# Kernel optimization log

Measured on AMD Instinct MI355X. Metric: run time of the kernel, lower is better.

The kernel has to match this reference:

```python
import jax, jax.numpy as jnp
import numpy as np

DIM = 1024
NUM_HEADS = 16
HEAD_DIM = DIM // NUM_HEADS
SCALING = HEAD_DIM ** (-0.5)


def setup_inputs() -> dict:
    key = jax.random.key(0)
    ks = jax.random.split(key, 9)
    B, S = 2, 2048
    s = DIM ** -0.5  # ~ torch Linear init scale
    inp = {
        "x": jax.random.normal(ks[0], (B, S, DIM), dtype=jnp.float32),
        "wq": jax.random.uniform(ks[1], (DIM, DIM), jnp.float32, -s, s),
        "bq": jax.random.uniform(ks[2], (DIM,), jnp.float32, -s, s),
        "wk": jax.random.uniform(ks[3], (DIM, DIM), jnp.float32, -s, s),
        "bk": jax.random.uniform(ks[4], (DIM,), jnp.float32, -s, s),
        "wv": jax.random.uniform(ks[5], (DIM, DIM), jnp.float32, -s, s),
        "bv": jax.random.uniform(ks[6], (DIM,), jnp.float32, -s, s),
        "wo": jax.random.uniform(ks[7], (DIM, DIM), jnp.float32, -s, s),
        "bo": jax.random.uniform(ks[8], (DIM,), jnp.float32, -s, s),
    }
    return inp


def reference(x, wq, bq, wk, bk, wv, bv, wo, bo):
    B, S, D = x.shape
    # projections (weights stored [out,in] like torch Linear -> x @ W.T + b)
    q = (x @ wq.T + bq).reshape(B, S, NUM_HEADS, HEAD_DIM)
    k = (x @ wk.T + bk).reshape(B, S, NUM_HEADS, HEAD_DIM)
    v = (x @ wv.T + bv).reshape(B, S, NUM_HEADS, HEAD_DIM)
    # [B,H,S,S] scores, scaled
    scores = jnp.einsum("bqhd,bkhd->bhqk", q, k) * SCALING
    attn = jax.nn.softmax(scores, axis=-1)
    # dropout p=0.0 (eval): identity
    out = jnp.einsum("bhqk,bkhd->bqhd", attn, v).reshape(B, S, D)
    return out @ wo.T + bo
```

## Files before the change

kernel.cpp:

```cpp
#include <hip/hip_runtime.h>

#define DIM 1024
#define NHEADS 16
#define HDIM 64
#define BATCH 2
#define SEQ 2048
#define MTOT (BATCH*SEQ)
#define QSCALE 0.18033688011112042f
#define XN ((size_t)MTOT*DIM)
#define WN ((size_t)DIM*DIM)

typedef __attribute__((ext_vector_type(8))) short short8;
typedef __attribute__((ext_vector_type(4))) float f32x4;
typedef __attribute__((ext_vector_type(16))) float f32x16;
typedef __attribute__((ext_vector_type(2))) int int2v;

static __device__ __forceinline__ unsigned short bf16rne(float f) {
    unsigned u = __builtin_bit_cast(unsigned, f);
    return (unsigned short)((u + 0x7fffu + ((u >> 16) & 1u)) >> 16);
}

static __device__ __forceinline__ void gld16(const void* g, void* l) {
    __builtin_amdgcn_global_load_lds((const __attribute__((address_space(1))) void*)g,
                                     (__attribute__((address_space(3))) void*)l, 16, 0, 0);
}

static __device__ __forceinline__ f32x16 mfma32(short8 a, short8 b, f32x16 c) {
    return __builtin_amdgcn_mfma_f32_32x32x16_bf16(a, b, c, 0, 0, 0);
}

__global__ __launch_bounds__(256)
void prep(const float* __restrict__ x, const float* __restrict__ wq, const float* __restrict__ wk,
          const float* __restrict__ wv, const float* __restrict__ wo, unsigned short* __restrict__ dst)
{
    const size_t i = ((size_t)blockIdx.x*256 + threadIdx.x)*8;
    const float* s; size_t o;
    if (i < XN)           { s = x;  o = i; }
    else if (i < XN+WN)   { s = wq; o = i - XN; }
    else if (i < XN+2*WN) { s = wk; o = i - XN - WN; }
    else if (i < XN+3*WN) { s = wv; o = i - XN - 2*WN; }
    else                  { s = wo; o = i - XN - 3*WN; }
    float4 a = *(const float4*)(s + o);
    float4 b = *(const float4*)(s + o + 4);
    uint4 w;
    w.x = (unsigned)bf16rne(a.x) | ((unsigned)bf16rne(a.y) << 16);
    w.y = (unsigned)bf16rne(a.z) | ((unsigned)bf16rne(a.w) << 16);
    w.z = (unsigned)bf16rne(b.x) | ((unsigned)bf16rne(b.y) << 16);
    w.w = (unsigned)bf16rne(b.z) | ((unsigned)bf16rne(b.w) << 16);
    *(uint4*)&dst[i] = w;
}

__global__ __launch_bounds__(256)
void gemm_qkv(const unsigned short* __restrict__ A,
              const unsigned short* __restrict__ W0, const unsigned short* __restrict__ W1,
              const unsigned short* __restrict__ W2,
              const float* __restrict__ b0, const float* __restrict__ b1, const float* __restrict__ b2,
              unsigned short* __restrict__ o0, unsigned short* __restrict__ o1, unsigned short* __restrict__ o2)
{
    __shared__ __align__(16) unsigned short As[3][4096];
    __shared__ __align__(16) unsigned short Bs[3][4096];
    const int t = threadIdx.x, wid = t >> 6, lane = t & 63;
    const int lr = lane & 15, lg = lane >> 4;
    const int bid = blockIdx.y * 24 + blockIdx.x;
    const int swz = (bid & 7) * 96 + (bid >> 3);
    const int sx = swz % 24, sy = swz / 24;
    const int widx = sx >> 3;
    const int n0 = (sx & 7) << 7;
    const int m0 = sy << 7;
    const unsigned short* W = widx == 0 ? W0 : (widx == 1 ? W1 : W2);
    const float* bias        = widx == 0 ? b0 : (widx == 1 ? b1 : b2);
    const float scale        = widx == 0 ? QSCALE : 1.0f;
    unsigned short* out      = widx == 0 ? o0 : (widx == 1 ? o1 : o2);

    const int wm = wid >> 1, wn = wid & 1;
    const int f0 = 2*wid, f1 = f0 + 1;
    const unsigned short* Ag0 = A + (size_t)(m0 + f0*16 + lr)*DIM + lg*8;
    const unsigned short* Ag1 = A + (size_t)(m0 + f1*16 + lr)*DIM + lg*8;
    const unsigned short* Bg0 = W + (size_t)(n0 + f0*16 + lr)*DIM + lg*8;
    const unsigned short* Bg1 = W + (size_t)(n0 + f1*16 + lr)*DIM + lg*8;

    auto stage = [&](int tt, int slot) {
        const int ko = tt * 32;
        gld16(Ag0 + ko, &As[slot][f0*512]); gld16(Ag1 + ko, &As[slot][f1*512]);
        gld16(Bg0 + ko, &Bs[slot][f0*512]); gld16(Bg1 + ko, &Bs[slot][f1*512]);
    };

    f32x4 acc[4][4] = {};
    stage(0, 0); stage(1, 1);
    int c0 = 0, c1 = 1, c2 = 2;

    for (int it = 0; it < DIM/32; ++it) {
        if (it < DIM/32 - 2) { asm volatile("s_waitcnt vmcnt(4)" ::: "memory"); }
        else                 { asm volatile("s_waitcnt vmcnt(0)" ::: "memory"); }
        __builtin_amdgcn_s_barrier();
        short8 af[4], bf[4];
        #pragma unroll
        for (int i = 0; i < 4; ++i) af[i] = *(const short8*)&As[c0][(wm*4+i)*512 + lane*8];
        #pragma unroll
        for (int i = 0; i < 4; ++i) bf[i] = *(const short8*)&Bs[c0][(wn*4+i)*512 + lane*8];
        if (it + 2 < DIM/32) stage(it + 2, c2);
        __builtin_amdgcn_s_setprio(1);
        #pragma unroll
        for (int mb = 0; mb < 4; ++mb)
            #pragma unroll
            for (int nb = 0; nb < 4; ++nb)
                acc[mb][nb] = __builtin_amdgcn_mfma_f32_16x16x32_bf16(af[mb], bf[nb], acc[mb][nb], 0, 0, 0);
        __builtin_amdgcn_s_setprio(0);
        const int tmp = c0; c0 = c1; c1 = c2; c2 = tmp;
    }

    #pragma unroll
    for (int nb = 0; nb < 4; ++nb) {
        const int col = n0 + wn*64 + nb*16 + lr;
        const float bv = bias[col];
        #pragma unroll
        for (int mb = 0; mb < 4; ++mb) {
            #pragma unroll
            for (int j = 0; j < 4; ++j) {
                const int row = m0 + wm*64 + mb*16 + lg*4 + j;
                out[(size_t)row*DIM + col] = bf16rne((acc[mb][nb][j] + bv) * scale);
            }
        }
    }
}

__global__ __launch_bounds__(256)
void gemm_o(const unsigned short* __restrict__ A, const unsigned short* __restrict__ W,
            const float* __restrict__ bias, float* __restrict__ fo)
{
    __shared__ __align__(16) unsigned short As[3][2048];
    __shared__ __align__(16) unsigned short Bs[3][4096];
    const int t = threadIdx.x, wid = t >> 6, lane = t & 63;
    const int lr = lane & 15, lg = lane >> 4;
    const int bid = blockIdx.y * 8 + blockIdx.x;
    const int swz = (bid & 7) * 64 + (bid >> 3);
    const int n0 = (swz & 7) << 7;
    const int m0 = (swz >> 3) << 6;
    const int wm = wid >> 1, wn = wid & 1;

    const int fa = wid;
    const int g0 = 2*wid, g1 = g0 + 1;
    const unsigned short* Ag  = A + (size_t)(m0 + fa*16 + lr)*DIM + lg*8;
    const unsigned short* Bg0 = W + (size_t)(n0 + g0*16 + lr)*DIM + lg*8;
    const unsigned short* Bg1 = W + (size_t)(n0 + g1*16 + lr)*DIM + lg*8;

    auto stage = [&](int tt, int slot) {
        const int ko = tt * 32;
        gld16(Ag + ko, &As[slot][fa*512]);
        gld16(Bg0 + ko, &Bs[slot][g0*512]); gld16(Bg1 + ko, &Bs[slot][g1*512]);
    };

    f32x4 acc[2][4] = {};
    stage(0, 0); stage(1, 1);
    int c0 = 0, c1 = 1, c2 = 2;

    for (int it = 0; it < DIM/32; ++it) {
        if (it < DIM/32 - 2) { asm volatile("s_waitcnt vmcnt(3)" ::: "memory"); }
        else                 { asm volatile("s_waitcnt vmcnt(0)" ::: "memory"); }
        __builtin_amdgcn_s_barrier();
        short8 af[2], bf[4];
        #pragma unroll
        for (int i = 0; i < 2; ++i) af[i] = *(const short8*)&As[c0][(wm*2+i)*512 + lane*8];
        #pragma unroll
        for (int i = 0; i < 4; ++i) bf[i] = *(const short8*)&Bs[c0][(wn*4+i)*512 + lane*8];
        if (it + 2 < DIM/32) stage(it + 2, c2);
        __builtin_amdgcn_s_setprio(1);
        #pragma unroll
        for (int mb = 0; mb < 2; ++mb)
            #pragma unroll
            for (int nb = 0; nb < 4; ++nb)
                acc[mb][nb] = __builtin_amdgcn_mfma_f32_16x16x32_bf16(af[mb], bf[nb], acc[mb][nb], 0, 0, 0);
        __builtin_amdgcn_s_setprio(0);
        const int tmp = c0; c0 = c1; c1 = c2; c2 = tmp;
    }

    #pragma unroll
    for (int nb = 0; nb < 4; ++nb) {
        const int col = n0 + wn*64 + nb*16 + lr;
        const float bv = bias[col];
        #pragma unroll
        for (int mb = 0; mb < 2; ++mb) {
            #pragma unroll
            for (int j = 0; j < 4; ++j) {
                const int row = m0 + wm*32 + mb*16 + lg*4 + j;
                fo[(size_t)row*DIM + col] = acc[mb][nb][j] + bv;
            }
        }
    }
}

__global__ __launch_bounds__(256)
void pack_kv(const unsigned short* __restrict__ Kg, const unsigned short* __restrict__ V,
             unsigned short* __restrict__ Kp, unsigned short* __restrict__ Vp)
{
    __shared__ unsigned short tile[64][66];
    const int t  = threadIdx.x;
    const int st = blockIdx.x;
    const int bh = blockIdx.y;
    const int isV = blockIdx.z;
    const int b = bh >> 4, h = bh & 15;
    const unsigned short* src = isV ? V : Kg;
    unsigned short* dstb = (isV ? Vp : Kp) + ((size_t)bh*32 + st)*4096;
    const int sr = t >> 3;
    const int dc = (t & 7) * 8;

    #pragma unroll
    for (int r = 0; r < 2; ++r) {
        const int s = r*32 + sr;
        short8 v = *(const short8*)(src + (size_t)(b*SEQ + st*64 + s)*DIM + h*HDIM + dc);
        #pragma unroll
        for (int e = 0; e < 8; ++e) tile[s][dc + e] = (unsigned short)v[e];
    }
    __syncthreads();
    #pragma unroll
    for (int r = 0; r < 2; ++r) {
        const int idx = t + r*256;
        const int fr = idx >> 6, ln = idx & 63;
        short8 ov;
        if (isV) {
            const int s0 = (fr & 3)*16 + (ln >> 5)*8;
            const int d  = (fr >> 2)*32 + (ln & 31);
            #pragma unroll
            for (int e = 0; e < 8; ++e) ov[e] = (short)tile[s0 + e][d];
        } else {
            const int key = (fr >> 2)*32 + (ln & 31);
            const int d0  = (fr & 3)*16 + (ln >> 5)*8;
            #pragma unroll
            for (int e = 0; e < 8; ++e) ov[e] = (short)tile[key][d0 + e];
        }
        *(short8*)(dstb + fr*512 + ln*8) = ov;
    }
}

struct PA { short8 p[4]; };

static __device__ __forceinline__ PA softmax_pack(const f32x16& s0, const f32x16& s1, float& lsum) {
    float rsum = 0.f;
    unsigned pw0[4][2], pw1[4][2];
    #pragma unroll
    for (int r1 = 0; r1 < 4; ++r1)
        #pragma unroll
        for (int tt = 0; tt < 2; ++tt) {
            float pa_ = __builtin_amdgcn_exp2f(s0[4*r1+2*tt]);
            float pb_ = __builtin_amdgcn_exp2f(s0[4*r1+2*tt+1]);
            float pc_ = __builtin_amdgcn_exp2f(s1[4*r1+2*tt]);
            float pd_ = __builtin_amdgcn_exp2f(s1[4*r1+2*tt+1]);
            rsum += (pa_ + pb_) + (pc_ + pd_);
            asm("v_cvt_pk_bf16_f32 %0, %1, %2" : "=v"(pw0[r1][tt]) : "v"(pa_), "v"(pb_));
            asm("v_cvt_pk_bf16_f32 %0, %1, %2" : "=v"(pw1[r1][tt]) : "v"(pc_), "v"(pd_));
        }
    rsum += __shfl_xor(rsum, 32);
    lsum += rsum;
    PA r;
    #pragma unroll
    for (int ss = 0; ss < 4; ++ss) {
        union { short8 s8; unsigned u[4]; } pu;
        #pragma unroll
        for (int tt = 0; tt < 2; ++tt) {
            const unsigned a = (ss >> 1) ? pw1[2*(ss&1)][tt]   : pw0[2*(ss&1)][tt];
            const unsigned b = (ss >> 1) ? pw1[2*(ss&1)+1][tt] : pw0[2*(ss&1)+1][tt];
            int2v sw = __builtin_amdgcn_permlane32_swap((int)a, (int)b, false, false);
            pu.u[tt]     = (unsigned)sw[0];
            pu.u[2 + tt] = (unsigned)sw[1];
        }
        r.p[ss] = pu.s8;
    }
    return r;
}

__global__ __launch_bounds__(256)
void attn_mfma2(const unsigned short* __restrict__ Q, const unsigned short* __restrict__ Kp,
                const unsigned short* __restrict__ Vp, unsigned short* __restrict__ O)
{
    __shared__ __align__(16) unsigned short Ks[4][4096];
    __shared__ __align__(16) unsigned short Vs[4][4096];
    const int t = threadIdx.x, wid = t >> 6, lane = t & 63;
    const int l31 = lane & 31, h = lane >> 5;
    const int bid = blockIdx.y * 16 + blockIdx.x;
    const int swz = (bid & 7) * 64 + (bid >> 3);
    const int qt = swz & 15, bh = swz >> 4;
    const int b = bh >> 4, hh = bh & 15;
    const size_t qkbase = (size_t)b*SEQ*DIM + (size_t)hh*HDIM;
    const unsigned short* Qb = Q + qkbase;
    unsigned short*       Ob = O + qkbase;
    const int q0 = qt*128 + wid*32;

    short8 qf[4];
    #pragma unroll
    for (int ds = 0; ds < 4; ++ds)
        qf[ds] = *(const short8*)&Qb[(size_t)(q0 + l31)*DIM + ds*16 + h*8];

    const int f0 = 2*wid, f1 = f0 + 1;
    const unsigned short* Kg0 = Kp + (size_t)bh*32*4096 + f0*512 + lane*8;
    const unsigned short* Kg1 = Kg0 + 512;
    const unsigned short* Vg0 = Vp + (size_t)bh*32*4096 + f0*512 + lane*8;
    const unsigned short* Vg1 = Vg0 + 512;

    auto stage = [&](int tn) {
        const size_t ko = (size_t)tn * 4096;
        const int bb = tn & 3;
        gld16(Kg0 + ko, &Ks[bb][f0*512]); gld16(Kg1 + ko, &Ks[bb][f1*512]);
        gld16(Vg0 + ko, &Vs[bb][f0*512]); gld16(Vg1 + ko, &Vs[bb][f1*512]);
    };

    f32x16 ctx0 = {}, ctx1 = {};
    float lsum = 0.0f;

    stage(0); stage(1);

    const int NW = SEQ/128;
    for (int w = 0; w < NW; ++w) {
        const int t0 = 2*w;
        const int ba = t0 & 3, bb2 = (t0+1) & 3;
        const bool more = (w + 1 < NW);

        if (more) { asm volatile("s_waitcnt vmcnt(4)" ::: "memory"); }
        else      { asm volatile("s_waitcnt vmcnt(0)" ::: "memory"); }
        __builtin_amdgcn_s_barrier();
        if (more) stage(t0 + 2);

        f32x16 s0a = {}, s1a = {};
        __builtin_amdgcn_s_setprio(1);
        #pragma unroll
        for (int ds = 0; ds < 4; ++ds) {
            short8 kf0 = *(const short8*)&Ks[ba][ds*512 + lane*8];
            short8 kf1 = *(const short8*)&Ks[ba][(4+ds)*512 + lane*8];
            s0a = mfma32(kf0, qf[ds], s0a);
            s1a = mfma32(kf1, qf[ds], s1a);
        }
        __builtin_amdgcn_s_setprio(0);

        PA pa = softmax_pack(s0a, s1a, lsum);

        if (more) { asm volatile("s_waitcnt vmcnt(4)" ::: "memory"); }
        else      { asm volatile("s_waitcnt vmcnt(0)" ::: "memory"); }
        __builtin_amdgcn_s_barrier();
        if (more) stage(t0 + 3);

        f32x16 s0b = {}, s1b = {};
        __builtin_amdgcn_s_setprio(1);
        #pragma unroll
        for (int ds = 0; ds < 4; ++ds) {
            short8 kf0 = *(const short8*)&Ks[bb2][ds*512 + lane*8];
            short8 kf1 = *(const short8*)&Ks[bb2][(4+ds)*512 + lane*8];
            s0b = mfma32(kf0, qf[ds], s0b);
            s1b = mfma32(kf1, qf[ds], s1b);
        }
        #pragma unroll
        for (int ss = 0; ss < 4; ++ss) {
            short8 vf0 = *(const short8*)&Vs[ba][ss*512 + lane*8];
            short8 vf1 = *(const short8*)&Vs[ba][(4+ss)*512 + lane*8];
            ctx0 = mfma32(pa.p[ss], vf0, ctx0);
            ctx1 = mfma32(pa.p[ss], vf1, ctx1);
        }
        __builtin_amdgcn_s_setprio(0);

        PA pb = softmax_pack(s0b, s1b, lsum);

        __builtin_amdgcn_s_setprio(1);
        #pragma unroll
        for (int ss = 0; ss < 4; ++ss) {
            short8 vf0 = *(const short8*)&Vs[bb2][ss*512 + lane*8];
            short8 vf1 = *(const short8*)&Vs[bb2][(4+ss)*512 + lane*8];
            ctx0 = mfma32(pb.p[ss], vf0, ctx0);
            ctx1 = mfma32(pb.p[ss], vf1, ctx1);
        }
        __builtin_amdgcn_s_setprio(0);
    }

    const float linv = 1.0f / lsum;
    #pragma unroll
    for (int r = 0; r < 16; ++r) {
        const int qrow = (r&3) + 8*(r>>2) + 4*h;
        const float nm = __shfl(linv, qrow);
        unsigned short* p = &Ob[(size_t)(q0 + qrow)*DIM + l31];
        p[0]  = bf16rne(ctx0[r] * nm);
        p[32] = bf16rne(ctx1[r] * nm);
    }
}

extern "C" void kernel_launch(void* const* d_in, const int* in_sizes, int n_in,
                              void* d_out, int out_size, void* d_ws, size_t ws_size,
                              hipStream_t stream) {
    const float* x  = (const float*)d_in[0];
    const float* wq = (const float*)d_in[1];
    const float* bq = (const float*)d_in[2];
    const float* wk = (const float*)d_in[3];
    const float* bk = (const float*)d_in[4];
    const float* wv = (const float*)d_in[5];
    const float* bv = (const float*)d_in[6];
    const float* wo = (const float*)d_in[7];
    const float* bo = (const float*)d_in[8];
    float* out = (float*)d_out;

    unsigned short* Xb  = (unsigned short*)d_ws;
    unsigned short* Wqb = Xb  + XN;
    unsigned short* Wkb = Wqb + WN;
    unsigned short* Wvb = Wkb + WN;
    unsigned short* Wob = Wvb + WN;
    unsigned short* Qb  = Wob + WN;
    unsigned short* Kb  = Qb  + XN;
    unsigned short* Vb  = Kb  + XN;
    unsigned short* Vpb = Vb  + XN;
    unsigned short* Kpb = Xb;
    unsigned short* Cb  = Vb;

    prep<<<4096, 256, 0, stream>>>(x, wq, wk, wv, wo, Xb);

    gemm_qkv<<<dim3(24, 32), 256, 0, stream>>>(Xb, Wqb, Wkb, Wvb, bq, bk, bv, Qb, Kb, Vb);

    pack_kv<<<dim3(SEQ/64, BATCH*NHEADS, 2), 256, 0, stream>>>(Kb, Vb, Kpb, Vpb);
    attn_mfma2<<<dim3(SEQ/128, BATCH*NHEADS), 256, 0, stream>>>(Qb, Kpb, Vpb, Cb);

    gemm_o<<<dim3(8, 64), 256, 0, stream>>>(Cb, Wob, bo, out);
}
```

Measured before the change: 139.7 us.

## Split attention over two key halves and merge partials in a combine kernel

The attention kernel now splits the key/value sequence into two halves along a new grid z-dimension. Each block writes unnormalized bf16 partial contexts and row sums to workspace. A new combine kernel adds the two partials, normalizes them and writes the context tensor for the output projection. This doubles the number of attention blocks to fill more of the GPU, at the cost of an extra launch and extra global traffic. The K/V staging also shrinks from four buffers to double buffering with a full vmcnt(0) wait each tile, which reduces load/compute overlap.

```diff
diff --git a/kernel.cpp b/kernel.cpp
--- a/kernel.cpp
+++ b/kernel.cpp
@@ -18,6 +18,9 @@
 static __device__ __forceinline__ unsigned short bf16rne(float f) {
     unsigned u = __builtin_bit_cast(unsigned, f);
     return (unsigned short)((u + 0x7fffu + ((u >> 16) & 1u)) >> 16);
+}
+static __device__ __forceinline__ float bf2f(unsigned short u) {
+    return __builtin_bit_cast(float, (unsigned)u << 16);
 }
 
 static __device__ __forceinline__ void gld16(const void* g, void* l) {
@@ -269,20 +272,20 @@
 }
 
 __global__ __launch_bounds__(256)
-void attn_mfma2(const unsigned short* __restrict__ Q, const unsigned short* __restrict__ Kp,
-                const unsigned short* __restrict__ Vp, unsigned short* __restrict__ O)
-{
-    __shared__ __align__(16) unsigned short Ks[4][4096];
-    __shared__ __align__(16) unsigned short Vs[4][4096];
+void attn_ks(const unsigned short* __restrict__ Q, const unsigned short* __restrict__ Kp,
+             const unsigned short* __restrict__ Vp,
+             unsigned short* __restrict__ Pc, float* __restrict__ Pl)
+{
+    __shared__ __align__(16) unsigned short Ks[2][4096];
+    __shared__ __align__(16) unsigned short Vs[2][4096];
     const int t = threadIdx.x, wid = t >> 6, lane = t & 63;
     const int l31 = lane & 31, h = lane >> 5;
     const int bid = blockIdx.y * 16 + blockIdx.x;
     const int swz = (bid & 7) * 64 + (bid >> 3);
     const int qt = swz & 15, bh = swz >> 4;
+    const int kz = blockIdx.z;
     const int b = bh >> 4, hh = bh & 15;
-    const size_t qkbase = (size_t)b*SEQ*DIM + (size_t)hh*HDIM;
-    const unsigned short* Qb = Q + qkbase;
-    unsigned short*       Ob = O + qkbase;
+    const unsigned short* Qb = Q + (size_t)b*SEQ*DIM + (size_t)hh*HDIM;
     const int q0 = qt*128 + wid*32;
 
     short8 qf[4];
@@ -291,92 +294,92 @@
         qf[ds] = *(const short8*)&Qb[(size_t)(q0 + l31)*DIM + ds*16 + h*8];
 
     const int f0 = 2*wid, f1 = f0 + 1;
-    const unsigned short* Kg0 = Kp + (size_t)bh*32*4096 + f0*512 + lane*8;
+    const size_t kvbase = (size_t)(bh*32 + kz*16)*4096;
+    const unsigned short* Kg0 = Kp + kvbase + f0*512 + lane*8;
     const unsigned short* Kg1 = Kg0 + 512;
-    const unsigned short* Vg0 = Vp + (size_t)bh*32*4096 + f0*512 + lane*8;
+    const unsigned short* Vg0 = Vp + kvbase + f0*512 + lane*8;
     const unsigned short* Vg1 = Vg0 + 512;
 
     auto stage = [&](int tn) {
         const size_t ko = (size_t)tn * 4096;
-        const int bb = tn & 3;
-        gld16(Kg0 + ko, &Ks[bb][f0*512]); gld16(Kg1 + ko, &Ks[bb][f1*512]);
-        gld16(Vg0 + ko, &Vs[bb][f0*512]); gld16(Vg1 + ko, &Vs[bb][f1*512]);
+        const int sl = tn & 1;
+        gld16(Kg0 + ko, &Ks[sl][f0*512]); gld16(Kg1 + ko, &Ks[sl][f1*512]);
+        gld16(Vg0 + ko, &Vs[sl][f0*512]); gld16(Vg1 + ko, &Vs[sl][f1*512]);
     };
 
     f32x16 ctx0 = {}, ctx1 = {};
     float lsum = 0.0f;
 
-    stage(0); stage(1);
-
-    const int NW = SEQ/128;
-    for (int w = 0; w < NW; ++w) {
-        const int t0 = 2*w;
-        const int ba = t0 & 3, bb2 = (t0+1) & 3;
-        const bool more = (w + 1 < NW);
-
-        if (more) { asm volatile("s_waitcnt vmcnt(4)" ::: "memory"); }
-        else      { asm volatile("s_waitcnt vmcnt(0)" ::: "memory"); }
+    stage(0);
+
+    for (int tn = 0; tn < 16; ++tn) {
+        const int sl = tn & 1;
+        asm volatile("s_waitcnt vmcnt(0)" ::: "memory");
         __builtin_amdgcn_s_barrier();
-        if (more) stage(t0 + 2);
-
-        f32x16 s0a = {}, s1a = {};
+        if (tn + 1 < 16) stage(tn + 1);
+
+        f32x16 s0 = {}, s1 = {};
         __builtin_amdgcn_s_setprio(1);
         #pragma unroll
         for (int ds = 0; ds < 4; ++ds) {
-            short8 kf0 = *(const short8*)&Ks[ba][ds*512 + lane*8];
-            short8 kf1 = *(const short8*)&Ks[ba][(4+ds)*512 + lane*8];
-            s0a = mfma32(kf0, qf[ds], s0a);
-            s1a = mfma32(kf1, qf[ds], s1a);
+            short8 kf0 = *(const short8*)&Ks[sl][ds*512 + lane*8];
+            short8 kf1 = *(const short8*)&Ks[sl][(4+ds)*512 + lane*8];
+            s0 = mfma32(kf0, qf[ds], s0);
+            s1 = mfma32(kf1, qf[ds], s1);
         }
         __builtin_amdgcn_s_setprio(0);
 
-        PA pa = softmax_pack(s0a, s1a, lsum);
-
-        if (more) { asm volatile("s_waitcnt vmcnt(4)" ::: "memory"); }
-        else      { asm volatile("s_waitcnt vmcnt(0)" ::: "memory"); }
-        __builtin_amdgcn_s_barrier();
-        if (more) stage(t0 + 3);
-
-        f32x16 s0b = {}, s1b = {};
+        PA pa = softmax_pack(s0, s1, lsum);
+
         __builtin_amdgcn_s_setprio(1);
         #pragma unroll
-        for (int ds = 0; ds < 4; ++ds) {
-            short8 kf0 = *(const short8*)&Ks[bb2][ds*512 + lane*8];
-            short8 kf1 = *(const short8*)&Ks[bb2][(4+ds)*512 + lane*8];
-            s0b = mfma32(kf0, qf[ds], s0b);
-            s1b = mfma32(kf1, qf[ds], s1b);
-        }
-        #pragma unroll
         for (int ss = 0; ss < 4; ++ss) {
-            short8 vf0 = *(const short8*)&Vs[ba][ss*512 + lane*8];
-            short8 vf1 = *(const short8*)&Vs[ba][(4+ss)*512 + lane*8];
+            short8 vf0 = *(const short8*)&Vs[sl][ss*512 + lane*8];
+            short8 vf1 = *(const short8*)&Vs[sl][(4+ss)*512 + lane*8];
             ctx0 = mfma32(pa.p[ss], vf0, ctx0);
             ctx1 = mfma32(pa.p[ss], vf1, ctx1);
         }
         __builtin_amdgcn_s_setprio(0);
-
-        PA pb = softmax_pack(s0b, s1b, lsum);
-
-        __builtin_amdgcn_s_setprio(1);
-        #pragma unroll
-        for (int ss = 0; ss < 4; ++ss) {
-            short8 vf0 = *(const short8*)&Vs[bb2][ss*512 + lane*8];
-            short8 vf1 = *(const short8*)&Vs[bb2][(4+ss)*512 + lane*8];
-            ctx0 = mfma32(pb.p[ss], vf0, ctx0);
-            ctx1 = mfma32(pb.p[ss], vf1, ctx1);
-        }
-        __builtin_amdgcn_s_setprio(0);
-    }
-
-    const float linv = 1.0f / lsum;
+    }
+
+    const size_t prow = ((size_t)kz*32 + bh)*SEQ + q0;
     #pragma unroll
     for (int r = 0; r < 16; ++r) {
         const int qrow = (r&3) + 8*(r>>2) + 4*h;
-        const float nm = __shfl(linv, qrow);
-        unsigned short* p = &Ob[(size_t)(q0 + qrow)*DIM + l31];
-        p[0]  = bf16rne(ctx0[r] * nm);
-        p[32] = bf16rne(ctx1[r] * nm);
-    }
+        unsigned short* p = &Pc[(prow + qrow)*64 + l31];
+        p[0]  = bf16rne(ctx0[r]);
+        p[32] = bf16rne(ctx1[r]);
+    }
+    if (lane < 32)
+        Pl[(size_t)kz*(32*SEQ) + (size_t)bh*SEQ + q0 + l31] = lsum;
+}
+
+__global__ __launch_bounds__(256)
+void combine(const unsigned short* __restrict__ Pc, const float* __restrict__ Pl,
+             unsigned short* __restrict__ Cb)
+{
+    const int i = blockIdx.x*256 + threadIdx.x;
+    const int row = i >> 3;
+    const int dc = (i & 7) * 8;
+    const float inv = 1.0f / (Pl[row] + Pl[32*SEQ + row]);
+    short8 a = *(const short8*)&Pc[(size_t)row*64 + dc];
+    short8 c = *(const short8*)&Pc[((size_t)32*SEQ + row)*64 + dc];
+    const int bh = row >> 11, s = row & (SEQ-1);
+    unsigned short* o = &Cb[((size_t)(bh>>4)*SEQ + s)*DIM + (bh&15)*HDIM + dc];
+    uint4 w;
+    float v0 = (bf2f((unsigned short)a[0]) + bf2f((unsigned short)c[0]))*inv;
+    float v1 = (bf2f((unsigned short)a[1]) + bf2f((unsigned short)c[1]))*inv;
+    float v2 = (bf2f((unsigned short)a[2]) + bf2f((unsigned short)c[2]))*inv;
+    float v3 = (bf2f((unsigned short)a[3]) + bf2f((unsigned short)c[3]))*inv;
+    float v4 = (bf2f((unsigned short)a[4]) + bf2f((unsigned short)c[4]))*inv;
+    float v5 = (bf2f((unsigned short)a[5]) + bf2f((unsigned short)c[5]))*inv;
+    float v6 = (bf2f((unsigned short)a[6]) + bf2f((unsigned short)c[6]))*inv;
+    float v7 = (bf2f((unsigned short)a[7]) + bf2f((unsigned short)c[7]))*inv;
+    w.x = (unsigned)bf16rne(v0) | ((unsigned)bf16rne(v1) << 16);
+    w.y = (unsigned)bf16rne(v2) | ((unsigned)bf16rne(v3) << 16);
+    w.z = (unsigned)bf16rne(v4) | ((unsigned)bf16rne(v5) << 16);
+    w.w = (unsigned)bf16rne(v6) | ((unsigned)bf16rne(v7) << 16);
+    *(uint4*)o = w;
 }
 
 extern "C" void kernel_launch(void* const* d_in, const int* in_sizes, int n_in,
@@ -403,14 +406,19 @@
     unsigned short* Vb  = Kb  + XN;
     unsigned short* Vpb = Vb  + XN;
     unsigned short* Kpb = Xb;
-    unsigned short* Cb  = Vb;
+    unsigned short* Pc  = Kb;
+    float*          Pl  = (float*)Wqb;
+    unsigned short* Cb  = Qb;
 
     prep<<<4096, 256, 0, stream>>>(x, wq, wk, wv, wo, Xb);
 
     gemm_qkv<<<dim3(24, 32), 256, 0, stream>>>(Xb, Wqb, Wkb, Wvb, bq, bk, bv, Qb, Kb, Vb);
 
     pack_kv<<<dim3(SEQ/64, BATCH*NHEADS, 2), 256, 0, stream>>>(Kb, Vb, Kpb, Vpb);
-    attn_mfma2<<<dim3(SEQ/128, BATCH*NHEADS), 256, 0, stream>>>(Qb, Kpb, Vpb, Cb);
+
+    attn_ks<<<dim3(16, BATCH*NHEADS, 2), 256, 0, stream>>>(Qb, Kpb, Vpb, Pc, Pl);
+
+    combine<<<2048, 256, 0, stream>>>(Pc, Pl, Cb);
 
     gemm_o<<<dim3(8, 64), 256, 0, stream>>>(Cb, Wob, bo, out);
 }
```

Result: slower. 149.2 us (+6.9%).

## Fuse K/V fragment packing into QKV GEMM epilogue via shared-memory transpose

Applied to the files above, without the earlier changes.

The QKV projection epilogue for K and V now stages the bias-added bf16 tile in shared memory, reusing the pipeline buffers. It then writes directly in the packed per-head fragment layout that the attention kernel consumes, so the separate pack_kv kernel is removed. This saves one launch and a full read and write of K and V through global memory. In exchange the GEMM epilogue gains two block barriers and strided, possibly bank-conflicting shared-memory reads, and the workspace aliasing changes so the attention output reuses the X buffer.

```diff
diff --git a/kernel.cpp b/kernel.cpp
--- a/kernel.cpp
+++ b/kernel.cpp
@@ -57,8 +57,9 @@
               const float* __restrict__ b0, const float* __restrict__ b1, const float* __restrict__ b2,
               unsigned short* __restrict__ o0, unsigned short* __restrict__ o1, unsigned short* __restrict__ o2)
 {
-    __shared__ __align__(16) unsigned short As[3][4096];
-    __shared__ __align__(16) unsigned short Bs[3][4096];
+    __shared__ __align__(16) unsigned short smem[24576];
+    #define AS(s) (smem + (s)*4096)
+    #define BS(s) (smem + 12288 + (s)*4096)
     const int t = threadIdx.x, wid = t >> 6, lane = t & 63;
     const int lr = lane & 15, lg = lane >> 4;
     const int bid = blockIdx.y * 24 + blockIdx.x;
@@ -69,8 +70,6 @@
     const int m0 = sy << 7;
     const unsigned short* W = widx == 0 ? W0 : (widx == 1 ? W1 : W2);
     const float* bias        = widx == 0 ? b0 : (widx == 1 ? b1 : b2);
-    const float scale        = widx == 0 ? QSCALE : 1.0f;
-    unsigned short* out      = widx == 0 ? o0 : (widx == 1 ? o1 : o2);
 
     const int wm = wid >> 1, wn = wid & 1;
     const int f0 = 2*wid, f1 = f0 + 1;
@@ -81,8 +80,8 @@
 
     auto stage = [&](int tt, int slot) {
         const int ko = tt * 32;
-        gld16(Ag0 + ko, &As[slot][f0*512]); gld16(Ag1 + ko, &As[slot][f1*512]);
-        gld16(Bg0 + ko, &Bs[slot][f0*512]); gld16(Bg1 + ko, &Bs[slot][f1*512]);
+        gld16(Ag0 + ko, AS(slot) + f0*512); gld16(Ag1 + ko, AS(slot) + f1*512);
+        gld16(Bg0 + ko, BS(slot) + f0*512); gld16(Bg1 + ko, BS(slot) + f1*512);
     };
 
     f32x4 acc[4][4] = {};
@@ -95,9 +94,9 @@
         __builtin_amdgcn_s_barrier();
         short8 af[4], bf[4];
         #pragma unroll
-        for (int i = 0; i < 4; ++i) af[i] = *(const short8*)&As[c0][(wm*4+i)*512 + lane*8];
-        #pragma unroll
-        for (int i = 0; i < 4; ++i) bf[i] = *(const short8*)&Bs[c0][(wn*4+i)*512 + lane*8];
+        for (int i = 0; i < 4; ++i) af[i] = *(const short8*)(AS(c0) + (wm*4+i)*512 + lane*8);
+        #pragma unroll
+        for (int i = 0; i < 4; ++i) bf[i] = *(const short8*)(BS(c0) + (wn*4+i)*512 + lane*8);
         if (it + 2 < DIM/32) stage(it + 2, c2);
         __builtin_amdgcn_s_setprio(1);
         #pragma unroll
@@ -109,19 +108,65 @@
         const int tmp = c0; c0 = c1; c1 = c2; c2 = tmp;
     }
 
-    #pragma unroll
-    for (int nb = 0; nb < 4; ++nb) {
-        const int col = n0 + wn*64 + nb*16 + lr;
-        const float bv = bias[col];
-        #pragma unroll
-        for (int mb = 0; mb < 4; ++mb) {
+    if (widx == 0) {
+        #pragma unroll
+        for (int nb = 0; nb < 4; ++nb) {
+            const int col = n0 + wn*64 + nb*16 + lr;
+            const float bv = bias[col];
             #pragma unroll
-            for (int j = 0; j < 4; ++j) {
-                const int row = m0 + wm*64 + mb*16 + lg*4 + j;
-                out[(size_t)row*DIM + col] = bf16rne((acc[mb][nb][j] + bv) * scale);
+            for (int mb = 0; mb < 4; ++mb) {
+                #pragma unroll
+                for (int j = 0; j < 4; ++j) {
+                    const int row = m0 + wm*64 + mb*16 + lg*4 + j;
+                    o0[(size_t)row*DIM + col] = bf16rne((acc[mb][nb][j] + bv) * QSCALE);
+                }
             }
         }
-    }
+    } else {
+        unsigned short* outp = (widx == 1) ? o1 : o2;
+        const int isV = (widx == 2);
+        __syncthreads();
+        unsigned short (*tile)[136] = (unsigned short (*)[136])smem;
+        #pragma unroll
+        for (int nb = 0; nb < 4; ++nb) {
+            const int col = wn*64 + nb*16 + lr;
+            const float bv = bias[n0 + col];
+            #pragma unroll
+            for (int mb = 0; mb < 4; ++mb) {
+                #pragma unroll
+                for (int j = 0; j < 4; ++j)
+                    tile[wm*64 + mb*16 + lg*4 + j][col] = bf16rne(acc[mb][nb][j] + bv);
+            }
+        }
+        __syncthreads();
+        const int bb  = m0 >> 11;
+        const int kt0 = (m0 & (SEQ-1)) >> 6;
+        const int hh0 = n0 >> 6;
+        #pragma unroll
+        for (int shot = 0; shot < 8; ++shot) {
+            const int idx = t + shot*256;
+            const int tid = idx >> 9;
+            const int fr  = (idx >> 6) & 7;
+            const int ln  = idx & 63;
+            const int ktl = tid & 1, hhl = tid >> 1;
+            short8 ov;
+            if (isV) {
+                const int r0 = ktl*64 + (fr & 3)*16 + (ln >> 5)*8;
+                const int c  = hhl*64 + (fr >> 2)*32 + (ln & 31);
+                #pragma unroll
+                for (int e = 0; e < 8; ++e) ov[e] = (short)tile[r0 + e][c];
+            } else {
+                const int r  = ktl*64 + (fr >> 2)*32 + (ln & 31);
+                const int cc = hhl*64 + (fr & 3)*16 + (ln >> 5)*8;
+                ov = *(const short8*)&tile[r][cc];
+            }
+            unsigned short* dst = outp
+                + ((size_t)((bb*NHEADS + hh0 + hhl)*32 + kt0 + ktl))*4096 + fr*512 + ln*8;
+            *(short8*)dst = ov;
+        }
+    }
+    #undef AS
+    #undef BS
 }
 
 __global__ __launch_bounds__(256)
@@ -186,49 +231,6 @@
                 fo[(size_t)row*DIM + col] = acc[mb][nb][j] + bv;
             }
         }
-    }
-}
-
-__global__ __launch_bounds__(256)
-void pack_kv(const unsigned short* __restrict__ Kg, const unsigned short* __restrict__ V,
-             unsigned short* __restrict__ Kp, unsigned short* __restrict__ Vp)
-{
-    __shared__ unsigned short tile[64][66];
-    const int t  = threadIdx.x;
-    const int st = blockIdx.x;
-    const int bh = blockIdx.y;
-    const int isV = blockIdx.z;
-    const int b = bh >> 4, h = bh & 15;
-    const unsigned short* src = isV ? V : Kg;
-    unsigned short* dstb = (isV ? Vp : Kp) + ((size_t)bh*32 + st)*4096;
-    const int sr = t >> 3;
-    const int dc = (t & 7) * 8;
-
-    #pragma unroll
-    for (int r = 0; r < 2; ++r) {
-        const int s = r*32 + sr;
-        short8 v = *(const short8*)(src + (size_t)(b*SEQ + st*64 + s)*DIM + h*HDIM + dc);
-        #pragma unroll
-        for (int e = 0; e < 8; ++e) tile[s][dc + e] = (unsigned short)v[e];
-    }
-    __syncthreads();
-    #pragma unroll
-    for (int r = 0; r < 2; ++r) {
-        const int idx = t + r*256;
-        const int fr = idx >> 6, ln = idx & 63;
-        short8 ov;
-        if (isV) {
-            const int s0 = (fr & 3)*16 + (ln >> 5)*8;
-            const int d  = (fr >> 2)*32 + (ln & 31);
-            #pragma unroll
-            for (int e = 0; e < 8; ++e) ov[e] = (short)tile[s0 + e][d];
-        } else {
-            const int key = (fr >> 2)*32 + (ln & 31);
-            const int d0  = (fr & 3)*16 + (ln >> 5)*8;
-            #pragma unroll
-            for (int e = 0; e < 8; ++e) ov[e] = (short)tile[key][d0 + e];
-        }
-        *(short8*)(dstb + fr*512 + ln*8) = ov;
     }
 }
 
@@ -399,17 +401,14 @@
     unsigned short* Wvb = Wkb + WN;
     unsigned short* Wob = Wvb + WN;
     unsigned short* Qb  = Wob + WN;
-    unsigned short* Kb  = Qb  + XN;
-    unsigned short* Vb  = Kb  + XN;
-    unsigned short* Vpb = Vb  + XN;
-    unsigned short* Kpb = Xb;
-    unsigned short* Cb  = Vb;
+    unsigned short* Kpb = Qb  + XN;
+    unsigned short* Vpb = Kpb + XN;
+    unsigned short* Cb  = Xb;
 
     prep<<<4096, 256, 0, stream>>>(x, wq, wk, wv, wo, Xb);
 
-    gemm_qkv<<<dim3(24, 32), 256, 0, stream>>>(Xb, Wqb, Wkb, Wvb, bq, bk, bv, Qb, Kb, Vb);
-
-    pack_kv<<<dim3(SEQ/64, BATCH*NHEADS, 2), 256, 0, stream>>>(Kb, Vb, Kpb, Vpb);
+    gemm_qkv<<<dim3(24, 32), 256, 0, stream>>>(Xb, Wqb, Wkb, Wvb, bq, bk, bv, Qb, Kpb, Vpb);
+
     attn_mfma2<<<dim3(SEQ/128, BATCH*NHEADS), 256, 0, stream>>>(Qb, Kpb, Vpb, Cb);
 
     gemm_o<<<dim3(8, 64), 256, 0, stream>>>(Cb, Wob, bo, out);
```

Result: faster. 133.2 us (-4.6%).
